# Optimization experiments

Hardware: AMD Instinct MI355X
Metric: run time of the kernel (lower is better)

Reference implementation:

```python
import jax, jax.numpy as jnp
import numpy as np

# Inner model dims (concrete MLP standing in for the wrapped keras model)
D_IN, HID, D_OUT = 1024, 2048, 10
POP, STD = 40, 0.1
S1 = D_IN * HID          # end of W1
S2 = S1 + HID            # end of b1
S3 = S2 + HID * D_OUT    # end of W2
N_PARAMS = S3 + D_OUT    # 2,119,690


def _flatten_weights(W1, b1, W2, b2):
    # tf.concat([reshape(w, [-1]) for w in trainable_weights])
    return jnp.concatenate([W1.reshape(-1), b1, W2.reshape(-1), b2])


def _mse_loss(flat_w, x, y):
    # expand_flat_trainable_weights + forward + compiled_loss (MSE)
    W1 = flat_w[:S1].reshape(D_IN, HID)
    b1 = flat_w[S1:S2]
    W2 = flat_w[S2:S3].reshape(HID, D_OUT)
    b2 = flat_w[S3:]
    pred = jax.nn.relu(x @ W1 + b1) @ W2 + b2
    return jnp.mean((pred - y) ** 2)


def _centered_ranks(t):
    # compute_centered_ranks: argsort-based ranks in [0, n), centered to [-0.5, 0.5]
    flat = t.reshape(-1)
    n = flat.shape[0]
    ranks = jnp.zeros((n,), jnp.float32).at[jnp.argsort(flat)].set(
        jnp.arange(n, dtype=jnp.float32))
    return (ranks / (n - 1) - 0.5).reshape(t.shape)


def setup_inputs() -> dict:
    key = jax.random.key(0)
    ks = jax.random.split(key, 5)
    return {
        "x": jax.random.normal(ks[0], (256, D_IN), jnp.float32),
        "y": jax.random.normal(ks[1], (256, D_OUT), jnp.float32),
        "W1": jax.random.normal(ks[2], (D_IN, HID), jnp.float32) * 0.02,
        "b1": jnp.zeros((HID,), jnp.float32),
        "W2": jax.random.normal(ks[3], (HID, D_OUT), jnp.float32) * 0.02,
        "b2": jnp.zeros((D_OUT,), jnp.float32),
        "noise": jax.random.normal(ks[4], (POP, N_PARAMS), jnp.float32),
    }


def reference(x, y, W1, b1, W2, b2, noise):
    flat_w = _flatten_weights(W1, b1, W2, b2)          # [N]
    eps = noise * STD                                   # stddev-scaled noise [POP, N]
    # parity: i even -> +1, i odd -> -1 (antithetic pairs)
    parity = jnp.array([1.0, -1.0], jnp.float32)
    perturbed = flat_w[None, None, :] + eps[:, None, :] * parity[None, :, None]  # [POP,2,N]
    # batched replacement for the pop_size*2 sequential forward passes
    losses = jax.vmap(jax.vmap(lambda w: _mse_loss(w, x, y)))(perturbed)  # [POP, 2]
    proc = _centered_ranks(losses)
    proc = proc[:, 0] - proc[:, 1]                      # [POP]
    grad = jnp.tensordot(eps, proc, axes=[[0], [0]]) / (POP * STD)  # [N]
    return grad
```

## Files before the change

kernel.cpp:

```cpp
#include <hip/hip_runtime.h>


#define NPLL 2119690LL
#define S1_  2097152
#define S2_  2099200
#define S3_  2119680

#define WS_PP   524288
#define WS_LOSS 3801088
#define WS_G    3801168
#define WS_XF   3801216
#define WW_PP   524288
#define WW_LOSS 7077888
#define WW_G    7077968
#define WW_XF   7078016
#define WW_NEED_BYTES 28836352ull

typedef _Float16 f16;
typedef __fp16   fp16x2 __attribute__((ext_vector_type(2)));
typedef _Float16 f16x2t __attribute__((ext_vector_type(2)));
typedef _Float16 f16x8 __attribute__((ext_vector_type(8)));
typedef float    f32x4 __attribute__((ext_vector_type(4)));

__device__ __forceinline__ unsigned pk2r(float a, float b, float& ra, float& rb) {
  fp16x2 h = __builtin_amdgcn_cvt_pkrtz(a, b);
  ra = a - (float)h[0];
  rb = b - (float)h[1];
  return __builtin_bit_cast(unsigned, h);
}
__device__ __forceinline__ unsigned pk2(float a, float b) {
  fp16x2 h = __builtin_amdgcn_cvt_pkrtz(a, b);
  return __builtin_bit_cast(unsigned, h);
}
__device__ __forceinline__ unsigned packh(float a, float b) {
  f16x2t v = {(f16)a, (f16)b};
  return __builtin_bit_cast(unsigned, v);
}
__device__ __forceinline__ float unpk_lo(unsigned u) {
  return (float)__builtin_bit_cast(f16, (unsigned short)(u & 0xffffu));
}
__device__ __forceinline__ float unpk_hi(unsigned u) {
  return (float)__builtin_bit_cast(f16, (unsigned short)(u >> 16));
}

__global__ __launch_bounds__(256) void k_xsplit(const float* __restrict__ x,
                                                f16* __restrict__ xf) {
  const int idx = blockIdx.x * 256 + threadIdx.x;
  const int b  = idx >> 7;
  const int k8 = idx & 127;
  const int kt = k8 >> 2, qh = k8 & 3;
  const int bblk = b >> 4, lm = b & 15;
  float4 a0 = *(const float4*)&x[(size_t)b * 1024 + k8 * 8];
  float4 a1 = *(const float4*)&x[(size_t)b * 1024 + k8 * 8 + 4];
  uint4 H;
  H.x = packh(a0.x, a0.y);
  H.y = packh(a0.z, a0.w);
  H.z = packh(a1.x, a1.y);
  H.w = packh(a1.z, a1.w);
  f16* dst = &xf[(((size_t)(kt * 16 + bblk) * 4 + qh) * 16 + lm) * 8];
  *(uint4*)dst = H;
}

__global__ __launch_bounds__(256) void k_base(const float* __restrict__ x,
                                              const float* __restrict__ W1,
                                              const float* __restrict__ b1,
                                              float* __restrict__ base) {
  constexpr int STR = 72;
  __shared__ float xsm[32 * STR];
  __shared__ float es[32 * STR];
  const int t  = threadIdx.x;
  const int j0 = blockIdx.x * 64;
  const int b0 = blockIdx.y * 32;
  const int tj = t & 15;
  const int tb = t >> 4;
  float acc[4][2] = {};
  for (int k0 = 0; k0 < 1024; k0 += 32) {
    __syncthreads();
    {
      int bb = t >> 3, kq = t & 7;
      float4 v = *(const float4*)&x[(size_t)(b0 + bb) * 1024 + k0 + kq * 4];
      int kb = kq * 4;
      xsm[(kb + 0) * STR + bb] = v.x;
      xsm[(kb + 1) * STR + bb] = v.y;
      xsm[(kb + 2) * STR + bb] = v.z;
      xsm[(kb + 3) * STR + bb] = v.w;
    }
#pragma unroll
    for (int r = 0; r < 2; ++r) {
      int idx = t + r * 256;
      int k = idx >> 4, jq = idx & 15, col = jq * 4;
      float4 v = *(const float4*)&W1[(size_t)(k0 + k) * 2048 + j0 + col];
      *(float4*)&es[k * STR + col + 4 * (col >> 5)] = v;
    }
    __syncthreads();
#pragma unroll 8
    for (int k = 0; k < 32; ++k) {
      const int ce = tj * 4;
      float4 e = *(const float4*)&es[k * STR + ce + 4 * (ce >> 5)];
      float2 a = *(const float2*)&xsm[k * STR + tb * 2];
      acc[0][0] += e.x * a.x; acc[0][1] += e.x * a.y;
      acc[1][0] += e.y * a.x; acc[1][1] += e.y * a.y;
      acc[2][0] += e.z * a.x; acc[2][1] += e.z * a.y;
      acc[3][0] += e.w * a.x; acc[3][1] += e.w * a.y;
    }
  }
#pragma unroll
  for (int jj = 0; jj < 4; ++jj) {
    int j = j0 + tj * 4 + jj;
    float bv = b1[j];
    float2 o = make_float2(acc[jj][0] + bv, acc[jj][1] + bv);
    *(float2*)&base[(size_t)j * 256 + b0 + tb * 2] = o;
  }
}

__global__ __launch_bounds__(256, 2) void k_big32(const f16* __restrict__ xf,
                                                  const float* __restrict__ noise,
                                                  const float* __restrict__ W2,
                                                  const float* __restrict__ base,
                                                  unsigned* __restrict__ ppu) {
  __shared__ __align__(16) char smem[8192];
  float* w2l = (float*)smem;
  float* e2l = w2l + 320;
  float* e1l = e2l + 320;

  const int t    = threadIdx.x;
  const int jt   = blockIdx.x, p = blockIdx.y;
  const int j0   = jt * 32;
  const int wave = t >> 6, lane = t & 63;
  const int lm   = lane & 15, qh = lane >> 4;
  const int g4   = qh * 4;
  const int bw   = wave * 64;
  const size_t pN = (size_t)p * NPLL;
  const bool stager = (t < 128);
  const int srow = t & 31, sq = (t >> 5) & 3;
  const int sswz = (srow & 7) << 3;
  const int aswz = (lm & 7) << 3;

  f16* eA0 = (f16*)smem;
  f16* eA1 = (f16*)(smem + 4096);

  float veA[8], veB[8];
  f16x8 Ba[4], Bb[4];
  f32x4 acc[2][4];
#pragma unroll
  for (int a = 0; a < 2; ++a)
#pragma unroll
    for (int b = 0; b < 4; ++b) acc[a][b] = (f32x4){0.f, 0.f, 0.f, 0.f};

  const float* Ebase = noise + pN + (size_t)(sq * 8) * 2048 + j0 + srow;
  const int boff = (wave * 4) * 512 + qh * 128 + lm * 8;

  if (stager) {
#pragma unroll
    for (int d = 0; d < 8; ++d) veA[d] = Ebase[(size_t)d * 2048];
#pragma unroll
    for (int d = 0; d < 8; ++d) veB[d] = Ebase[65536 + (size_t)d * 2048];
  }
#pragma unroll
  for (int nf = 0; nf < 4; ++nf)
    Ba[nf] = *(const f16x8*)&xf[boff + nf * 512];
#pragma unroll
  for (int nf = 0; nf < 4; ++nf)
    Bb[nf] = *(const f16x8*)&xf[8192 + boff + nf * 512];

#define KSTEP32(EAC, VE, BF, KS)                                               \
  do {                                                                         \
    if (stager) {                                                              \
      float r0, r1, r2, r3, r4, r5, r6, r7;                                    \
      uint4 H, L;                                                              \
      H.x = pk2r(VE[0], VE[1], r0, r1);                                        \
      H.y = pk2r(VE[2], VE[3], r2, r3);                                        \
      H.z = pk2r(VE[4], VE[5], r4, r5);                                        \
      H.w = pk2r(VE[6], VE[7], r6, r7);                                        \
      *(uint4*)&EAC[srow * 64 + ((sq * 8) ^ sswz)] = H;                        \
      L.x = pk2(r0, r1); L.y = pk2(r2, r3);                                    \
      L.z = pk2(r4, r5); L.w = pk2(r6, r7);                                    \
      *(uint4*)&EAC[srow * 64 + (((sq + 4) * 8) ^ sswz)] = L;                  \
      if ((KS) + 2 < 32) {                                                     \
        const float* En = Ebase + (size_t)((KS) + 2) * 65536;                  \
        _Pragma("unroll") for (int d = 0; d < 8; ++d)                          \
          VE[d] = En[(size_t)d * 2048];                                        \
      }                                                                        \
    }                                                                          \
    asm volatile("s_waitcnt lgkmcnt(0)" ::: "memory");     \
    __builtin_amdgcn_s_barrier();                        \
    asm volatile("" ::: "memory");                                             \
    _Pragma("unroll") for (int mf = 0; mf < 2; ++mf) {                         \
      const int ra = mf * 16 + lm;                                             \
      f16x8 Ah = *(const f16x8*)&EAC[ra * 64 + ((qh * 8) ^ aswz)];             \
      f16x8 Al = *(const f16x8*)&EAC[ra * 64 + (((qh + 4) * 8) ^ aswz)];       \
      _Pragma("unroll") for (int nf = 0; nf < 4; ++nf) {                       \
        acc[mf][nf] = __builtin_amdgcn_mfma_f32_16x16x32_f16(Ah, BF[nf], acc[mf][nf], 0, 0, 0); \
        acc[mf][nf] = __builtin_amdgcn_mfma_f32_16x16x32_f16(Al, BF[nf], acc[mf][nf], 0, 0, 0); \
      }                                                                        \
    }                                                                          \
    if ((KS) + 2 < 32) {                                                       \
      const f16* xn = xf + (size_t)((KS) + 2) * 8192;                          \
      _Pragma("unroll") for (int nf = 0; nf < 4; ++nf)                         \
        BF[nf] = *(const f16x8*)&xn[boff + nf * 512];                          \
    }                                                                          \
  } while (0)

  for (int ks = 0; ks < 32; ks += 2) {
    KSTEP32(eA0, veA, Ba, ks);
    KSTEP32(eA1, veB, Bb, ks + 1);
  }
#undef KSTEP32

  __syncthreads();
  for (int i = t; i < 320; i += 256) {
    w2l[i] = W2[j0 * 10 + i];
    e2l[i] = noise[pN + S2_ + (size_t)j0 * 10 + i];
  }
  if (t < 32) e1l[t] = noise[pN + S1_ + j0 + t];
  __syncthreads();

#pragma unroll 1
  for (int s = 0; s < 2; ++s) {
    const float sf = s ? -0.1f : 0.1f;
#pragma unroll 1
    for (int nf = 0; nf < 4; ++nf) {
      const int bl = bw + nf * 16 + lm;
      float ppv[10];
#pragma unroll
      for (int o = 0; o < 10; ++o) ppv[o] = 0.f;
#pragma unroll
      for (int mf = 0; mf < 2; ++mf)
#pragma unroll
        for (int r = 0; r < 4; ++r) {
          const int jl = mf * 16 + g4 + r;
          const float bs = base[(size_t)(j0 + jl) * 256 + bl];
          const float h =
              fmaxf(fmaf(sf, acc[mf][nf][r] + e1l[jl], bs), 0.f);
#pragma unroll
          for (int o = 0; o < 10; ++o)
            ppv[o] = fmaf(h, fmaf(sf, e2l[jl * 10 + o], w2l[jl * 10 + o]),
                          ppv[o]);
        }
#pragma unroll
      for (int o = 0; o < 10; ++o) {
        float v = ppv[o];
        v += __shfl_xor(v, 16, 64);
        v += __shfl_xor(v, 32, 64);
        ppv[o] = v;
      }
      if (lane < 16) {
        const size_t u0 = ((((size_t)p * 2 + s) * 64 + jt) * 256 + bl) * 5;
        ppu[u0 + 0] = packh(ppv[0], ppv[1]);
        ppu[u0 + 1] = packh(ppv[2], ppv[3]);
        ppu[u0 + 2] = packh(ppv[4], ppv[5]);
        ppu[u0 + 3] = packh(ppv[6], ppv[7]);
        ppu[u0 + 4] = packh(ppv[8], ppv[9]);
      }
    }
  }
}

__global__ __launch_bounds__(256) void k_big64(const f16* __restrict__ xf,
                                               const float* __restrict__ noise,
                                               const float* __restrict__ W2,
                                               const float* __restrict__ base,
                                               unsigned* __restrict__ ppu) {
  __shared__ __align__(16) char smem[16384];
  float* w2l = (float*)smem;
  float* e2l = w2l + 640;
  float* e1l = e2l + 640;

  const int t    = threadIdx.x;
  const int jt   = blockIdx.x, p = blockIdx.y;
  const int j0   = jt * 64;
  const int wave = t >> 6, lane = t & 63;
  const int lm   = lane & 15, qh = lane >> 4;
  const int g4   = qh * 4;
  const int bw   = wave * 64;
  const size_t pN = (size_t)p * NPLL;
  const int srow = t & 63, sq = t >> 6;
  const int sswz = (srow & 7) << 3;
  const int aswz = (lm & 7) << 3;

  f16* eA0 = (f16*)smem;
  f16* eA1 = (f16*)(smem + 8192);

  float veA[8], veB[8];
  f16x8 Ba[4], Bb[4];
  f32x4 acc[4][4];
#pragma unroll
  for (int a = 0; a < 4; ++a)
#pragma unroll
    for (int b = 0; b < 4; ++b) acc[a][b] = (f32x4){0.f, 0.f, 0.f, 0.f};

  const float* Ebase = noise + pN + (size_t)(sq * 8) * 2048 + j0 + srow;
  const int boff = (wave * 4) * 512 + qh * 128 + lm * 8;

#pragma unroll
  for (int d = 0; d < 8; ++d) veA[d] = Ebase[(size_t)d * 2048];
#pragma unroll
  for (int nf = 0; nf < 4; ++nf)
    Ba[nf] = *(const f16x8*)&xf[boff + nf * 512];
#pragma unroll
  for (int d = 0; d < 8; ++d) veB[d] = Ebase[65536 + (size_t)d * 2048];
#pragma unroll
  for (int nf = 0; nf < 4; ++nf)
    Bb[nf] = *(const f16x8*)&xf[8192 + boff + nf * 512];

#define KSTEP64(EAC, VE, BF, KS)                                               \
  do {                                                                         \
    {                                                                          \
      float r0, r1, r2, r3, r4, r5, r6, r7;                                    \
      uint4 H, L;                                                              \
      H.x = pk2r(VE[0], VE[1], r0, r1);                                        \
      H.y = pk2r(VE[2], VE[3], r2, r3);                                        \
      H.z = pk2r(VE[4], VE[5], r4, r5);                                        \
      H.w = pk2r(VE[6], VE[7], r6, r7);                                        \
      *(uint4*)&EAC[srow * 64 + ((sq * 8) ^ sswz)] = H;                        \
      L.x = pk2(r0, r1); L.y = pk2(r2, r3);                                    \
      L.z = pk2(r4, r5); L.w = pk2(r6, r7);                                    \
      *(uint4*)&EAC[srow * 64 + (((sq + 4) * 8) ^ sswz)] = L;                  \
    }                                                                          \
    if ((KS) + 2 < 32) {                                                       \
      const float* En = Ebase + (size_t)((KS) + 2) * 65536;                    \
      _Pragma("unroll") for (int d = 0; d < 8; ++d)                            \
        VE[d] = En[(size_t)d * 2048];                                          \
    }                                                                          \
    asm volatile("s_waitcnt lgkmcnt(0)" ::: "memory");                         \
    __builtin_amdgcn_s_barrier();                                              \
    asm volatile("" ::: "memory");                                             \
    _Pragma("unroll") for (int mf = 0; mf < 4; ++mf) {                         \
      const int ra = mf * 16 + lm;                                             \
      f16x8 Ah = *(const f16x8*)&EAC[ra * 64 + ((qh * 8) ^ aswz)];             \
      f16x8 Al = *(const f16x8*)&EAC[ra * 64 + (((qh + 4) * 8) ^ aswz)];       \
      _Pragma("unroll") for (int nf = 0; nf < 4; ++nf) {                       \
        acc[mf][nf] = __builtin_amdgcn_mfma_f32_16x16x32_f16(Ah, BF[nf], acc[mf][nf], 0, 0, 0); \
        acc[mf][nf] = __builtin_amdgcn_mfma_f32_16x16x32_f16(Al, BF[nf], acc[mf][nf], 0, 0, 0); \
      }                                                                        \
    }                                                                          \
    if ((KS) + 2 < 32) {                                                       \
      const f16* xn = xf + (size_t)((KS) + 2) * 8192;                          \
      _Pragma("unroll") for (int nf = 0; nf < 4; ++nf)                         \
        BF[nf] = *(const f16x8*)&xn[boff + nf * 512];                          \
    }                                                                          \
  } while (0)

  for (int ks = 0; ks < 32; ks += 2) {
    KSTEP64(eA0, veA, Ba, ks);
    KSTEP64(eA1, veB, Bb, ks + 1);
  }
#undef KSTEP64

  __syncthreads();
  for (int i = t; i < 640; i += 256) {
    w2l[i] = W2[j0 * 10 + i];
    e2l[i] = noise[pN + S2_ + (size_t)j0 * 10 + i];
  }
  if (t < 64) e1l[t] = noise[pN + S1_ + j0 + t];
  __syncthreads();

#pragma unroll 1
  for (int s = 0; s < 2; ++s) {
    const float sf = s ? -0.1f : 0.1f;
    float ppv[4][10];
#pragma unroll
    for (int nf = 0; nf < 4; ++nf)
#pragma unroll
      for (int o = 0; o < 10; ++o) ppv[nf][o] = 0.f;
#pragma unroll
    for (int mf = 0; mf < 4; ++mf)
#pragma unroll
      for (int r = 0; r < 4; ++r) {
        const int jl = mf * 16 + g4 + r;
        const float e1v = e1l[jl];
        float w2s[10];
#pragma unroll
        for (int o = 0; o < 10; ++o)
          w2s[o] = fmaf(sf, e2l[jl * 10 + o], w2l[jl * 10 + o]);
#pragma unroll
        for (int nf = 0; nf < 4; ++nf) {
          const float bs = base[(size_t)(j0 + jl) * 256 + bw + nf * 16 + lm];
          const float h = fmaxf(fmaf(sf, acc[mf][nf][r] + e1v, bs), 0.f);
#pragma unroll
          for (int o = 0; o < 10; ++o) ppv[nf][o] = fmaf(h, w2s[o], ppv[nf][o]);
        }
      }
#pragma unroll
    for (int nf = 0; nf < 4; ++nf)
#pragma unroll
      for (int o = 0; o < 10; ++o) {
        float v = ppv[nf][o];
        v += __shfl_xor(v, 16, 64);
        v += __shfl_xor(v, 32, 64);
        ppv[nf][o] = v;
      }
    if (lane < 16) {
#pragma unroll
      for (int nf = 0; nf < 4; ++nf) {
        const int bl = bw + nf * 16 + lm;
        const size_t u0 = ((((size_t)p * 2 + s) * 32 + jt) * 256 + bl) * 5;
        ppu[u0 + 0] = packh(ppv[nf][0], ppv[nf][1]);
        ppu[u0 + 1] = packh(ppv[nf][2], ppv[nf][3]);
        ppu[u0 + 2] = packh(ppv[nf][4], ppv[nf][5]);
        ppu[u0 + 3] = packh(ppv[nf][6], ppv[nf][7]);
        ppu[u0 + 4] = packh(ppv[nf][8], ppv[nf][9]);
      }
    }
  }
}

__global__ __launch_bounds__(256) void k_loss(const unsigned* __restrict__ ppu,
                                              const float* __restrict__ y,
                                              const float* __restrict__ b2,
                                              const float* __restrict__ noise,
                                              float* __restrict__ loss,
                                              int JT) {
  const int b = threadIdx.x;
  const int p = blockIdx.x >> 1, s = blockIdx.x & 1;
  const float sf = s ? -0.1f : 0.1f;
  const size_t pN = (size_t)p * NPLL;
  float pred[10];
#pragma unroll
  for (int o = 0; o < 10; ++o) pred[o] = b2[o] + sf * noise[pN + S3_ + o];
  for (int jt = 0; jt < JT; ++jt) {
    const size_t u0 = ((((size_t)p * 2 + s) * JT + jt) * 256 + b) * 5;
#pragma unroll
    for (int q = 0; q < 5; ++q) {
      unsigned u = ppu[u0 + q];
      pred[2 * q]     += unpk_lo(u);
      pred[2 * q + 1] += unpk_hi(u);
    }
  }
  float e = 0.f;
#pragma unroll
  for (int o = 0; o < 10; ++o) {
    float d = pred[o] - y[b * 10 + o];
    e += d * d;
  }
  __shared__ float red[256];
  red[b] = e;
  __syncthreads();
  for (int st = 128; st > 0; st >>= 1) {
    if (b < st) red[b] += red[b + st];
    __syncthreads();
  }
  if (b == 0) loss[blockIdx.x] = red[0] * (1.0f / 2560.0f);
}

__global__ void k_rank(const float* __restrict__ loss, float* __restrict__ g) {
  __shared__ float ls[80];
  __shared__ float rk[80];
  const int t = threadIdx.x;
  if (t < 80) ls[t] = loss[t];
  __syncthreads();
  if (t < 80) {
    float li = ls[t];
    int r = 0;
    for (int j = 0; j < 80; ++j) {
      float lj = ls[j];
      r += (lj < li) || (lj == li && j < t);
    }
    rk[t] = (float)r;
  }
  __syncthreads();
  if (t < 40) g[t] = (rk[2 * t] - rk[2 * t + 1]) * (1.0f / (79.0f * 40.0f));
}

__global__ __launch_bounds__(256) void k_grad(const float* __restrict__ noise,
                                              const float* __restrict__ g,
                                              float* __restrict__ out) {
  __shared__ float gg[40];
  const int t = threadIdx.x;
  if (t < 40) gg[t] = g[t];
  __syncthreads();
  const long long NH = NPLL / 2;
  long long idx = (long long)blockIdx.x * 256 + t;
  if (idx >= NH) return;
  float2 a = make_float2(0.f, 0.f);
#pragma unroll 8
  for (int p = 0; p < 40; ++p) {
    float2 v = *(const float2*)&noise[(size_t)p * NPLL + idx * 2];
    a.x += v.x * gg[p];
    a.y += v.y * gg[p];
  }
  *(float2*)&out[idx * 2] = a;
}

extern "C" void kernel_launch(void* const* d_in, const int* in_sizes, int n_in,
                              void* d_out, int out_size, void* d_ws, size_t ws_size,
                              hipStream_t stream) {
  const float* x     = (const float*)d_in[0];
  const float* y     = (const float*)d_in[1];
  const float* W1    = (const float*)d_in[2];
  const float* b1    = (const float*)d_in[3];
  const float* W2    = (const float*)d_in[4];
  const float* b2    = (const float*)d_in[5];
  const float* noise = (const float*)d_in[6];
  float* out  = (float*)d_out;
  float* ws   = (float*)d_ws;
  float* base = ws;

  const bool wide = (ws_size >= WW_NEED_BYTES);
  unsigned* ppu = (unsigned*)(ws + (wide ? WW_PP : WS_PP));
  float* loss = ws + (wide ? WW_LOSS : WS_LOSS);
  float* g    = ws + (wide ? WW_G : WS_G);
  f16* xf     = (f16*)(ws + (wide ? WW_XF : WS_XF));

  k_xsplit<<<128, 256, 0, stream>>>(x, xf);
  k_base<<<dim3(32, 8), 256, 0, stream>>>(x, W1, b1, base);
  if (wide)
    k_big32<<<dim3(64, 40), 256, 0, stream>>>(xf, noise, W2, base, ppu);
  else
    k_big64<<<dim3(32, 40), 256, 0, stream>>>(xf, noise, W2, base, ppu);
  k_loss<<<80, 256, 0, stream>>>(ppu, y, b2, noise, loss, wide ? 64 : 32);
  k_rank<<<1, 128, 0, stream>>>(loss, g);
  k_grad<<<4141, 256, 0, stream>>>(noise, g, out);
}
```

Measured before the change: 340.2 us.

## Spread noise staging across all threads and deepen noise prefetch to four steps

The noise-tile staging into LDS used to run on only half the block (128 threads, 8 floats each). It now runs on all 256 threads with 4 floats each, writing uint2 halves at swizzled offsets. The global prefetch of noise moves from two k-steps ahead to four, using four register buffers with the k-loop unrolled by 4. This is meant to spread load issue across all waves and hide more global-load latency, at the cost of extra registers under launch_bounds(256,2).

```diff
diff --git a/kernel.cpp b/kernel.cpp
--- a/kernel.cpp
+++ b/kernel.cpp
@@ -131,15 +131,16 @@
   const int g4   = qh * 4;
   const int bw   = wave * 64;
   const size_t pN = (size_t)p * NPLL;
-  const bool stager = (t < 128);
-  const int srow = t & 31, sq = (t >> 5) & 3;
-  const int sswz = (srow & 7) << 3;
+  const int srow = t & 31, sq = t >> 5;
+  const int sr7 = srow & 7, cq = sq >> 1, hh = (sq & 1) * 4;
+  const int hiOff = ((cq ^ sr7) << 3) + hh;
+  const int loOff = (((cq + 4) ^ sr7) << 3) + hh;
   const int aswz = (lm & 7) << 3;
 
   f16* eA0 = (f16*)smem;
   f16* eA1 = (f16*)(smem + 4096);
 
-  float veA[8], veB[8];
+  float veA[4], veB[4], veC[4], veD[4];
   f16x8 Ba[4], Bb[4];
   f32x4 acc[2][4];
 #pragma unroll
@@ -147,15 +148,17 @@
 #pragma unroll
     for (int b = 0; b < 4; ++b) acc[a][b] = (f32x4){0.f, 0.f, 0.f, 0.f};
 
-  const float* Ebase = noise + pN + (size_t)(sq * 8) * 2048 + j0 + srow;
+  const float* Ebase = noise + pN + (size_t)(sq * 4) * 2048 + j0 + srow;
   const int boff = (wave * 4) * 512 + qh * 128 + lm * 8;
 
-  if (stager) {
-#pragma unroll
-    for (int d = 0; d < 8; ++d) veA[d] = Ebase[(size_t)d * 2048];
-#pragma unroll
-    for (int d = 0; d < 8; ++d) veB[d] = Ebase[65536 + (size_t)d * 2048];
-  }
+#pragma unroll
+  for (int d = 0; d < 4; ++d) veA[d] = Ebase[(size_t)d * 2048];
+#pragma unroll
+  for (int d = 0; d < 4; ++d) veB[d] = Ebase[65536 + (size_t)d * 2048];
+#pragma unroll
+  for (int d = 0; d < 4; ++d) veC[d] = Ebase[131072 + (size_t)d * 2048];
+#pragma unroll
+  for (int d = 0; d < 4; ++d) veD[d] = Ebase[196608 + (size_t)d * 2048];
 #pragma unroll
   for (int nf = 0; nf < 4; ++nf)
     Ba[nf] = *(const f16x8*)&xf[boff + nf * 512];
@@ -165,22 +168,19 @@
 
 #define KSTEP32(EAC, VE, BF, KS)                                               \
   do {                                                                         \
-    if (stager) {                                                              \
-      float r0, r1, r2, r3, r4, r5, r6, r7;                                    \
-      uint4 H, L;                                                              \
+    {     \
+      float r0, r1, r2, r3;                                                    \
+      uint2 H, L;                                                              \
       H.x = pk2r(VE[0], VE[1], r0, r1);                                        \
       H.y = pk2r(VE[2], VE[3], r2, r3);                                        \
-      H.z = pk2r(VE[4], VE[5], r4, r5);                                        \
-      H.w = pk2r(VE[6], VE[7], r6, r7);                                        \
-      *(uint4*)&EAC[srow * 64 + ((sq * 8) ^ sswz)] = H;                        \
+      *(uint2*)&EAC[srow * 64 + hiOff] = H;                                    \
       L.x = pk2(r0, r1); L.y = pk2(r2, r3);                                    \
-      L.z = pk2(r4, r5); L.w = pk2(r6, r7);                                    \
-      *(uint4*)&EAC[srow * 64 + (((sq + 4) * 8) ^ sswz)] = L;                  \
-      if ((KS) + 2 < 32) {                                                     \
-        const float* En = Ebase + (size_t)((KS) + 2) * 65536;                  \
-        _Pragma("unroll") for (int d = 0; d < 8; ++d)                          \
-          VE[d] = En[(size_t)d * 2048];                                        \
-      }                                                                        \
+      *(uint2*)&EAC[srow * 64 + loOff] = L;                                    \
+    }                                                                          \
+    if ((KS) + 4 < 32) {                 \
+      const float* En = Ebase + (size_t)((KS) + 4) * 65536;                    \
+      _Pragma("unroll") for (int d = 0; d < 4; ++d)                            \
+        VE[d] = En[(size_t)d * 2048];                                          \
     }                                                                          \
     asm volatile("s_waitcnt lgkmcnt(0)" ::: "memory");     \
     __builtin_amdgcn_s_barrier();                        \
@@ -194,16 +194,18 @@
         acc[mf][nf] = __builtin_amdgcn_mfma_f32_16x16x32_f16(Al, BF[nf], acc[mf][nf], 0, 0, 0); \
       }                                                                        \
     }                                                                          \
-    if ((KS) + 2 < 32) {                                                       \
+    if ((KS) + 2 < 32) {      \
       const f16* xn = xf + (size_t)((KS) + 2) * 8192;                          \
       _Pragma("unroll") for (int nf = 0; nf < 4; ++nf)                         \
         BF[nf] = *(const f16x8*)&xn[boff + nf * 512];                          \
     }                                                                          \
   } while (0)
 
-  for (int ks = 0; ks < 32; ks += 2) {
+  for (int ks = 0; ks < 32; ks += 4) {
     KSTEP32(eA0, veA, Ba, ks);
     KSTEP32(eA1, veB, Bb, ks + 1);
+    KSTEP32(eA0, veC, Ba, ks + 2);
+    KSTEP32(eA1, veD, Bb, ks + 3);
   }
 #undef KSTEP32
 
```

Measured after the change: 336.1 us. About the same (-1.2%).
